# Kernel optimization log

Hardware: AMD Instinct MI355X
Metric: run time of the kernel (lower is better)

Reference implementation:

```python
import jax, jax.numpy as jnp
import numpy as np

H = 16  # num_heads
D = 64  # head_dim


def setup_inputs() -> dict:
    key = jax.random.key(0)
    ks = jax.random.split(key, 9)
    B, S, E = 2, 2048, 1024
    scale = 1.0 / np.sqrt(E)
    return {
        "hidden_states": jax.random.normal(ks[0], (B, S, E), jnp.float32),
        "bias": jax.random.normal(ks[1], (1, H, S, S), jnp.float32) * 0.02,
        "Wq": jax.random.normal(ks[2], (E, E), jnp.float32) * scale,
        "bq": jax.random.normal(ks[3], (E,), jnp.float32) * 0.02,
        "Wk": jax.random.normal(ks[4], (E, E), jnp.float32) * scale,
        "bk": jax.random.normal(ks[5], (E,), jnp.float32) * 0.02,
        "Wv": jax.random.normal(ks[6], (E, E), jnp.float32) * scale,
        "bv": jax.random.normal(ks[7], (E,), jnp.float32) * 0.02,
        "Wo": jax.random.normal(ks[8], (E, E), jnp.float32) * scale,
    }


def _split_heads(x, B, S):
    # (B, S, E) -> (B, H, S, D)
    return x.reshape(B, S, H, D).transpose(0, 2, 1, 3)


def reference(hidden_states, bias, Wq, bq, Wk, bk, Wv, bv, Wo):
    B, S, E = hidden_states.shape
    # nn.Linear: y = x @ W^T + b
    q = _split_heads(hidden_states @ Wq.T + bq, B, S)
    k = _split_heads(hidden_states @ Wk.T + bk, B, S)
    v = _split_heads(hidden_states @ Wv.T + bv, B, S)
    scores = jnp.einsum("bhqd,bhkd->bhqk", q, k) / jnp.sqrt(jnp.asarray(D, q.dtype))
    scores = scores + bias  # bias [1,H,S,S] broadcasts over batch (matches .repeat)
    attn = jax.nn.softmax(scores, axis=-1)
    out = jnp.einsum("bhqk,bhkd->bhqd", attn, v)
    out = out.transpose(0, 2, 1, 3).reshape(B, S, E)
    return out @ Wo.T
```

## Files before the change

kernel.cpp:

```cpp
#include <hip/hip_runtime.h>
#include <hip/hip_bf16.h>


typedef __attribute__((ext_vector_type(8))) __bf16 bf16x8;
typedef __attribute__((ext_vector_type(4))) float f32x4;

__device__ __forceinline__ void gl2lds16(const void* g, void* l) {
    __builtin_amdgcn_global_load_lds(
        (const __attribute__((address_space(1))) void*)g,
        (__attribute__((address_space(3))) void*)l, 16, 0, 0);
}

__global__ __launch_bounds__(256) void prep(
    const float* __restrict__ hs, const float* __restrict__ Wq,
    const float* __restrict__ Wk, const float* __restrict__ Wv,
    const float* __restrict__ Wo,
    __bf16* __restrict__ hsb, __bf16* __restrict__ wqb, __bf16* __restrict__ wkb,
    __bf16* __restrict__ wvb, __bf16* __restrict__ wohb, __bf16* __restrict__ wolb)
{
    size_t i = (size_t)blockIdx.x * 256 + threadIdx.x;
    const float* s; __bf16 *d1, *d2 = nullptr; size_t off;
    if (i < 1048576)      { s = hs; d1 = hsb; off = i; }
    else if (i < 1310720) { s = Wq; d1 = wqb; off = i - 1048576; }
    else if (i < 1572864) { s = Wk; d1 = wkb; off = i - 1310720; }
    else if (i < 1835008) { s = Wv; d1 = wvb; off = i - 1572864; }
    else                  { s = Wo; d1 = wohb; d2 = wolb; off = i - 1835008; }
    float4 v = *(const float4*)(s + off * 4);
    union { __bf16 b[4]; uint2 u; } ph;
    ph.b[0] = (__bf16)v.x; ph.b[1] = (__bf16)v.y;
    ph.b[2] = (__bf16)v.z; ph.b[3] = (__bf16)v.w;
    *(uint2*)(d1 + off * 4) = ph.u;
    if (d2) {
        union { __bf16 b[4]; uint2 u; } pl;
        pl.b[0] = (__bf16)(v.x - (float)ph.b[0]);
        pl.b[1] = (__bf16)(v.y - (float)ph.b[1]);
        pl.b[2] = (__bf16)(v.z - (float)ph.b[2]);
        pl.b[3] = (__bf16)(v.w - (float)ph.b[3]);
        *(uint2*)(d2 + off * 4) = pl.u;
    }
}

__global__ __launch_bounds__(256, 3) void gemm_qkv(
    const __bf16* __restrict__ hsb, const __bf16* __restrict__ wqb,
    const __bf16* __restrict__ wkb, const __bf16* __restrict__ wvb,
    const float* __restrict__ bq, const float* __restrict__ bk, const float* __restrict__ bv,
    __bf16* __restrict__ qo, __bf16* __restrict__ ko, __bf16* __restrict__ vTo)
{
    __shared__ alignas(16) __bf16 As[128][32];
    __shared__ alignas(16) __bf16 Ws[128][32];
    const int tid = threadIdx.x;
    const int w = tid >> 6, lane = tid & 63, quad = lane >> 4, l = lane & 15;
    const int blk = blockIdx.x;
    const int proj = blk >> 8;
    const int loc = blk & 255;
    int bm, bn;
    const __bf16 *Ap, *Wp; const float* bp;
    if (proj == 0)      { Ap = hsb; Wp = wqb; bp = bq; bm = (loc >> 3) << 7; bn = (loc & 7) << 7; }
    else if (proj == 1) { Ap = hsb; Wp = wkb; bp = bk; bm = (loc >> 3) << 7; bn = (loc & 7) << 7; }
    else                { Ap = wvb; Wp = hsb; bp = bv; bm = (loc & 7) << 7; bn = (loc >> 3) << 7; }
    const int wm = (w >> 1) << 6, wn = (w & 1) << 6;
    const int seg_r = lane >> 2, seg_c = (lane & 3) << 3;

    f32x4 acc[4][4];
#pragma unroll
    for (int i = 0; i < 4; ++i)
#pragma unroll
        for (int j = 0; j < 4; ++j) acc[i][j] = f32x4{0.f, 0.f, 0.f, 0.f};

    for (int k0 = 0; k0 < 1024; k0 += 32) {
        __syncthreads();
#pragma unroll
        for (int j = 0; j < 2; ++j) {
            int seg = w * 2 + j;
            int row = seg * 16 + seg_r;
            gl2lds16(Ap + (size_t)(bm + row) * 1024 + k0 + seg_c,
                     (char*)As + seg * 1024 + lane * 16);
            gl2lds16(Wp + (size_t)(bn + row) * 1024 + k0 + seg_c,
                     (char*)Ws + seg * 1024 + lane * 16);
        }
        __syncthreads();
        bf16x8 af[4], bfr[4];
#pragma unroll
        for (int t = 0; t < 4; ++t) {
            af[t]  = *(const bf16x8*)&As[wm + t * 16 + l][quad * 8];
            bfr[t] = *(const bf16x8*)&Ws[wn + t * 16 + l][quad * 8];
        }
#pragma unroll
        for (int mt = 0; mt < 4; ++mt)
#pragma unroll
            for (int nt = 0; nt < 4; ++nt)
                acc[mt][nt] = __builtin_amdgcn_mfma_f32_16x16x32_bf16(
                    af[mt], bfr[nt], acc[mt][nt], 0, 0, 0);
    }

    if (proj < 2) {
        __bf16* dst = proj ? ko : qo;
        const float scale = proj ? 1.0f : 0.125f;
        float bcol[4];
#pragma unroll
        for (int nt = 0; nt < 4; ++nt) bcol[nt] = bp[bn + wn + nt * 16 + l];
#pragma unroll
        for (int mt = 0; mt < 4; ++mt)
#pragma unroll
            for (int r = 0; r < 4; ++r) {
                int m = bm + wm + mt * 16 + quad * 4 + r;
                int b_ = m >> 11, s = m & 2047;
#pragma unroll
                for (int nt = 0; nt < 4; ++nt) {
                    int n = bn + wn + nt * 16 + l;
                    int h = n >> 6, d = n & 63;
                    dst[(((size_t)(b_ * 16 + h) * 2048 + s) << 6) + d] =
                        (__bf16)((acc[mt][nt][r] + bcol[nt]) * scale);
                }
            }
    } else {
#pragma unroll
        for (int mt = 0; mt < 4; ++mt)
#pragma unroll
            for (int r = 0; r < 4; ++r) {
                int im = bm + wm + mt * 16 + quad * 4 + r;
                int h = im >> 6, d = im & 63;
                float bm_ = bp[im];
#pragma unroll
                for (int nt = 0; nt < 4; ++nt) {
                    int in = bn + wn + nt * 16 + l;
                    int b_ = in >> 11, s = in & 2047;
                    vTo[(((size_t)(b_ * 16 + h) * 64 + d) << 11) + s] =
                        (__bf16)(acc[mt][nt][r] + bm_);
                }
            }
    }
}

__global__ __launch_bounds__(256, 2) void flash_attn_mfma(
    const __bf16* __restrict__ q, const __bf16* __restrict__ k,
    const __bf16* __restrict__ vT, const float* __restrict__ bias,
    __bf16* __restrict__ attn_hi, __bf16* __restrict__ attn_lo)
{
    constexpr int S = 2048;
    constexpr int NT = S / 64;
    __shared__ alignas(16) unsigned char smem[50176];
    __bf16 (*Ps)[68] = (__bf16(*)[68])(smem + 32768);

    const int tid = threadIdx.x;
    const int b = blockIdx.x, h = blockIdx.y, qt = blockIdx.z;
    const int bh = b * 16 + h;
    const int q0 = qt * 128;
    const int w = tid >> 6, lane = tid & 63, quad = lane >> 4, l = lane & 15;

    const __bf16* Kp0 = k + (size_t)bh * S * 64;
    const __bf16* Vp0 = vT + (size_t)bh * 64 * S;
    const float*  Bp0 = bias + (size_t)h * S * S + (size_t)q0 * S;

    {
        const __bf16* Qp = q + ((size_t)bh * S + q0) * 64;
#pragma unroll
        for (int j = 0; j < 4; ++j) {
            int P = (w * 4 + j) * 64 + lane;
            int row = P >> 3, pblk = P & 7;
            int lblk = pblk ^ (row & 7);
            gl2lds16(Qp + row * 64 + lblk * 8, (char*)smem + 32768 + (size_t)P * 16);
        }
#pragma unroll
        for (int j = 0; j < 2; ++j) {
            int P = (w * 2 + j) * 64 + lane;
            int row = P >> 3, pblk = P & 7;
            int lblk = pblk ^ (row & 7);
            gl2lds16(Kp0 + row * 64 + lblk * 8,        (char*)smem + (size_t)P * 16);
            gl2lds16(Vp0 + (size_t)row * S + lblk * 8, (char*)smem + 16384 + (size_t)P * 16);
        }
    }

    f32x4 pf[2][4];
#pragma unroll
    for (int rt = 0; rt < 2; ++rt)
#pragma unroll
        for (int r = 0; r < 4; ++r) {
            const float* bp = Bp0 + (size_t)(w * 32 + rt * 16 + quad * 4 + r) * S + l;
#pragma unroll
            for (int ct = 0; ct < 4; ++ct) pf[rt][ct][r] = bp[ct * 16];
        }

    __syncthreads();

    bf16x8 qf[2][2];
    {
        const __bf16 (*Qs)[64] = (const __bf16(*)[64])(smem + 32768);
#pragma unroll
        for (int rt = 0; rt < 2; ++rt)
#pragma unroll
            for (int ks = 0; ks < 2; ++ks) {
                int row = w * 32 + rt * 16 + l;
                qf[rt][ks] = *(const bf16x8*)&Qs[row][((ks * 4 + quad) ^ (row & 7)) * 8];
            }
    }
    __syncthreads();

    float l_[2][4];
    f32x4 o_[2][4];
#pragma unroll
    for (int rt = 0; rt < 2; ++rt)
#pragma unroll
        for (int r = 0; r < 4; ++r) {
            l_[rt][r] = 0.0f;
            o_[rt][r] = f32x4{0.f, 0.f, 0.f, 0.f};
        }

    for (int kt = 0; kt < NT; ++kt) {
        const int cur = kt & 1;
        const __bf16 (*Ks)[64]  = (const __bf16(*)[64])(smem + cur * 8192);
        const __bf16 (*VTs)[64] = (const __bf16(*)[64])(smem + 16384 + cur * 8192);

        f32x4 sc[2][4];
#pragma unroll
        for (int rt = 0; rt < 2; ++rt)
#pragma unroll
            for (int ct = 0; ct < 4; ++ct) sc[rt][ct] = pf[rt][ct];

        if (kt + 1 < NT) {
            const __bf16* Kt = Kp0 + (kt + 1) * 64 * 64;
            const __bf16* Vt = Vp0 + (kt + 1) * 64;
            char* Kd = (char*)smem + (cur ^ 1) * 8192;
            char* Vd = (char*)smem + 16384 + (cur ^ 1) * 8192;
#pragma unroll
            for (int j = 0; j < 2; ++j) {
                int P = (w * 2 + j) * 64 + lane;
                int row = P >> 3, pblk = P & 7;
                int lblk = pblk ^ (row & 7);
                gl2lds16(Kt + row * 64 + lblk * 8,        Kd + (size_t)P * 16);
                gl2lds16(Vt + (size_t)row * S + lblk * 8, Vd + (size_t)P * 16);
            }
            const float* Bn = Bp0 + (kt + 1) * 64;
#pragma unroll
            for (int rt = 0; rt < 2; ++rt)
#pragma unroll
                for (int r = 0; r < 4; ++r) {
                    const float* bp = Bn + (size_t)(w * 32 + rt * 16 + quad * 4 + r) * S + l;
#pragma unroll
                    for (int ct = 0; ct < 4; ++ct) pf[rt][ct][r] = bp[ct * 16];
                }
        }

        __builtin_amdgcn_s_setprio(1);
#pragma unroll
        for (int ct = 0; ct < 4; ++ct) {
            int krow = ct * 16 + l;
            bf16x8 b0 = *(const bf16x8*)&Ks[krow][((0 + quad) ^ (l & 7)) * 8];
            bf16x8 b1 = *(const bf16x8*)&Ks[krow][((4 + quad) ^ (l & 7)) * 8];
            sc[0][ct] = __builtin_amdgcn_mfma_f32_16x16x32_bf16(qf[0][0], b0, sc[0][ct], 0, 0, 0);
            sc[0][ct] = __builtin_amdgcn_mfma_f32_16x16x32_bf16(qf[0][1], b1, sc[0][ct], 0, 0, 0);
            sc[1][ct] = __builtin_amdgcn_mfma_f32_16x16x32_bf16(qf[1][0], b0, sc[1][ct], 0, 0, 0);
            sc[1][ct] = __builtin_amdgcn_mfma_f32_16x16x32_bf16(qf[1][1], b1, sc[1][ct], 0, 0, 0);
        }
        __builtin_amdgcn_s_setprio(0);

#pragma unroll
        for (int rt = 0; rt < 2; ++rt)
#pragma unroll
            for (int r = 0; r < 4; ++r) {
                int row = w * 32 + rt * 16 + quad * 4 + r;
                float ps = 0.f;
#pragma unroll
                for (int ct = 0; ct < 4; ++ct) {
                    float p = __expf(sc[rt][ct][r] - 8.0f);
                    Ps[row][ct * 16 + l] = (__bf16)p;
                    ps += p;
                }
                l_[rt][r] += ps;
            }

        __builtin_amdgcn_s_setprio(1);
#pragma unroll
        for (int ks = 0; ks < 2; ++ks) {
            bf16x8 pa0 = *(const bf16x8*)&Ps[w * 32 + l][ks * 32 + quad * 8];
            bf16x8 pa1 = *(const bf16x8*)&Ps[w * 32 + 16 + l][ks * 32 + quad * 8];
#pragma unroll
            for (int dt = 0; dt < 4; ++dt) {
                bf16x8 vb = *(const bf16x8*)&VTs[dt * 16 + l][((ks * 4 + quad) ^ (l & 7)) * 8];
                o_[0][dt] = __builtin_amdgcn_mfma_f32_16x16x32_bf16(pa0, vb, o_[0][dt], 0, 0, 0);
                o_[1][dt] = __builtin_amdgcn_mfma_f32_16x16x32_bf16(pa1, vb, o_[1][dt], 0, 0, 0);
            }
        }
        __builtin_amdgcn_s_setprio(0);

        __syncthreads();
    }

#pragma unroll
    for (int rt = 0; rt < 2; ++rt)
#pragma unroll
        for (int r = 0; r < 4; ++r) {
            float ps = l_[rt][r];
            ps += __shfl_xor(ps, 1);
            ps += __shfl_xor(ps, 2);
            ps += __shfl_xor(ps, 4);
            ps += __shfl_xor(ps, 8);
            float linv = 1.0f / ps;
            int row = q0 + w * 32 + rt * 16 + quad * 4 + r;
            size_t base = (size_t)(b * S + row) * 1024 + h * 64;
#pragma unroll
            for (int dt = 0; dt < 4; ++dt) {
                float x = o_[rt][dt][r] * linv;
                __bf16 hi = (__bf16)x;
                attn_hi[base + dt * 16 + l] = hi;
                attn_lo[base + dt * 16 + l] = (__bf16)(x - (float)hi);
            }
        }
}

__global__ __launch_bounds__(256, 3) void gemm_out(
    const __bf16* __restrict__ ah, const __bf16* __restrict__ al,
    const __bf16* __restrict__ wh, const __bf16* __restrict__ wl,
    float* __restrict__ C)
{
    __shared__ alignas(16) __bf16 Ah[64][32], Al[64][32];
    __shared__ alignas(16) __bf16 Wh[128][32], Wl[128][32];
    const int tid = threadIdx.x;
    const int w = tid >> 6, lane = tid & 63, quad = lane >> 4, l = lane & 15;
    const int bm = (int)(blockIdx.x >> 3) << 6;
    const int bn = (int)(blockIdx.x & 7) << 7;
    const int wm = (w >> 1) << 5, wn = (w & 1) << 6;
    const int seg_r = lane >> 2, seg_c = (lane & 3) << 3;

    f32x4 acc[2][4];
#pragma unroll
    for (int i = 0; i < 2; ++i)
#pragma unroll
        for (int j = 0; j < 4; ++j) acc[i][j] = f32x4{0.f, 0.f, 0.f, 0.f};

    for (int k0 = 0; k0 < 1024; k0 += 32) {
        __syncthreads();
        {
            int row = w * 16 + seg_r;
            gl2lds16(ah + (size_t)(bm + row) * 1024 + k0 + seg_c,
                     (char*)Ah + w * 1024 + lane * 16);
            gl2lds16(al + (size_t)(bm + row) * 1024 + k0 + seg_c,
                     (char*)Al + w * 1024 + lane * 16);
#pragma unroll
            for (int j = 0; j < 2; ++j) {
                int seg = w * 2 + j;
                int wrow = seg * 16 + seg_r;
                gl2lds16(wh + (size_t)(bn + wrow) * 1024 + k0 + seg_c,
                         (char*)Wh + seg * 1024 + lane * 16);
                gl2lds16(wl + (size_t)(bn + wrow) * 1024 + k0 + seg_c,
                         (char*)Wl + seg * 1024 + lane * 16);
            }
        }
        __syncthreads();
        bf16x8 ahf[2], alf[2], whf[4], wlf[4];
#pragma unroll
        for (int t = 0; t < 2; ++t) {
            ahf[t] = *(const bf16x8*)&Ah[wm + t * 16 + l][quad * 8];
            alf[t] = *(const bf16x8*)&Al[wm + t * 16 + l][quad * 8];
        }
#pragma unroll
        for (int t = 0; t < 4; ++t) {
            whf[t] = *(const bf16x8*)&Wh[wn + t * 16 + l][quad * 8];
            wlf[t] = *(const bf16x8*)&Wl[wn + t * 16 + l][quad * 8];
        }
#pragma unroll
        for (int mt = 0; mt < 2; ++mt)
#pragma unroll
            for (int nt = 0; nt < 4; ++nt) {
                acc[mt][nt] = __builtin_amdgcn_mfma_f32_16x16x32_bf16(ahf[mt], whf[nt], acc[mt][nt], 0, 0, 0);
                acc[mt][nt] = __builtin_amdgcn_mfma_f32_16x16x32_bf16(ahf[mt], wlf[nt], acc[mt][nt], 0, 0, 0);
                acc[mt][nt] = __builtin_amdgcn_mfma_f32_16x16x32_bf16(alf[mt], whf[nt], acc[mt][nt], 0, 0, 0);
            }
    }

#pragma unroll
    for (int mt = 0; mt < 2; ++mt)
#pragma unroll
        for (int r = 0; r < 4; ++r) {
            int m = bm + wm + mt * 16 + quad * 4 + r;
#pragma unroll
            for (int nt = 0; nt < 4; ++nt)
                C[(size_t)m * 1024 + bn + wn + nt * 16 + l] = acc[mt][nt][r];
        }
}

extern "C" void kernel_launch(void* const* d_in, const int* in_sizes, int n_in,
                              void* d_out, int out_size, void* d_ws, size_t ws_size,
                              hipStream_t stream) {
    const float* hs   = (const float*)d_in[0];
    const float* bias = (const float*)d_in[1];
    const float* Wq   = (const float*)d_in[2];
    const float* bq   = (const float*)d_in[3];
    const float* Wk   = (const float*)d_in[4];
    const float* bk   = (const float*)d_in[5];
    const float* Wv   = (const float*)d_in[6];
    const float* bv   = (const float*)d_in[7];
    const float* Wo   = (const float*)d_in[8];
    float* out = (float*)d_out;
    char* ws = (char*)d_ws;

    __bf16* attn_hi = (__bf16*)(ws);
    __bf16* attn_lo = (__bf16*)(ws + ((size_t) 8 << 20));
    __bf16* qb      = (__bf16*)(ws + ((size_t)16 << 20));
    __bf16* kb      = (__bf16*)(ws + ((size_t)24 << 20));
    __bf16* vTb     = (__bf16*)(ws + ((size_t)32 << 20));
    __bf16* hsb     = (__bf16*)(ws + ((size_t)40 << 20));
    __bf16* wqb     = (__bf16*)(ws + ((size_t)48 << 20));
    __bf16* wkb     = (__bf16*)(ws + ((size_t)50 << 20));
    __bf16* wvb     = (__bf16*)(ws + ((size_t)52 << 20));
    __bf16* wohb    = (__bf16*)(ws + ((size_t)54 << 20));
    __bf16* wolb    = (__bf16*)(ws + ((size_t)56 << 20));

    prep<<<8192, 256, 0, stream>>>(hs, Wq, Wk, Wv, Wo, hsb, wqb, wkb, wvb, wohb, wolb);

    gemm_qkv<<<768, 256, 0, stream>>>(hsb, wqb, wkb, wvb, bq, bk, bv, qb, kb, vTb);

    dim3 fg(2, 16, 16);
    flash_attn_mfma<<<fg, 256, 0, stream>>>(qb, kb, vTb, bias, attn_hi, attn_lo);

    gemm_out<<<512, 256, 0, stream>>>(attn_hi, attn_lo, wohb, wolb, out);
}
```

Baseline: 508.8 us.

## Process both batches per block to share bias tile loads in flash attention

```diff
diff --git a/kernel.cpp b/kernel.cpp
--- a/kernel.cpp
+++ b/kernel.cpp
@@ -140,167 +140,166 @@
     constexpr int S = 2048;
     constexpr int NT = S / 64;
     __shared__ alignas(16) unsigned char smem[50176];
-    __bf16 (*Ps)[68] = (__bf16(*)[68])(smem + 32768);
 
     const int tid = threadIdx.x;
-    const int b = blockIdx.x, h = blockIdx.y, qt = blockIdx.z;
-    const int bh = b * 16 + h;
-    const int q0 = qt * 128;
+    const int h = blockIdx.x, qt = blockIdx.y;
+    const int q0 = qt * 64;
     const int w = tid >> 6, lane = tid & 63, quad = lane >> 4, l = lane & 15;
 
-    const __bf16* Kp0 = k + (size_t)bh * S * 64;
-    const __bf16* Vp0 = vT + (size_t)bh * 64 * S;
-    const float*  Bp0 = bias + (size_t)h * S * S + (size_t)q0 * S;
-
-    {
-        const __bf16* Qp = q + ((size_t)bh * S + q0) * 64;
-#pragma unroll
-        for (int j = 0; j < 4; ++j) {
-            int P = (w * 4 + j) * 64 + lane;
-            int row = P >> 3, pblk = P & 7;
-            int lblk = pblk ^ (row & 7);
-            gl2lds16(Qp + row * 64 + lblk * 8, (char*)smem + 32768 + (size_t)P * 16);
-        }
+    const float* Bp0 = bias + (size_t)h * S * S + (size_t)q0 * S;
+
+#pragma unroll
+    for (int b = 0; b < 2; ++b) {
+        const __bf16* Qp = q + ((size_t)(b * 16 + h) * S + q0) * 64;
+        const __bf16* Kp = k + (size_t)(b * 16 + h) * S * 64;
+        const __bf16* Vp = vT + (size_t)(b * 16 + h) * 64 * S;
 #pragma unroll
         for (int j = 0; j < 2; ++j) {
             int P = (w * 2 + j) * 64 + lane;
             int row = P >> 3, pblk = P & 7;
             int lblk = pblk ^ (row & 7);
-            gl2lds16(Kp0 + row * 64 + lblk * 8,        (char*)smem + (size_t)P * 16);
-            gl2lds16(Vp0 + (size_t)row * S + lblk * 8, (char*)smem + 16384 + (size_t)P * 16);
-        }
-    }
-
-    f32x4 pf[2][4];
-#pragma unroll
-    for (int rt = 0; rt < 2; ++rt)
-#pragma unroll
-        for (int r = 0; r < 4; ++r) {
-            const float* bp = Bp0 + (size_t)(w * 32 + rt * 16 + quad * 4 + r) * S + l;
-#pragma unroll
-            for (int ct = 0; ct < 4; ++ct) pf[rt][ct][r] = bp[ct * 16];
-        }
+            gl2lds16(Qp + row * 64 + lblk * 8,
+                     (char*)smem + 32768 + b * 8192 + (size_t)P * 16);
+            gl2lds16(Kp + row * 64 + lblk * 8,
+                     (char*)smem + b * 8192 + (size_t)P * 16);
+            gl2lds16(Vp + (size_t)row * S + lblk * 8,
+                     (char*)smem + 16384 + b * 8192 + (size_t)P * 16);
+        }
+    }
+
+    f32x4 pf[4];
+#pragma unroll
+    for (int r = 0; r < 4; ++r) {
+        const float* bp = Bp0 + (size_t)(w * 16 + quad * 4 + r) * S + l;
+#pragma unroll
+        for (int ct = 0; ct < 4; ++ct) pf[ct][r] = bp[ct * 16];
+    }
 
     __syncthreads();
 
     bf16x8 qf[2][2];
-    {
-        const __bf16 (*Qs)[64] = (const __bf16(*)[64])(smem + 32768);
-#pragma unroll
-        for (int rt = 0; rt < 2; ++rt)
-#pragma unroll
-            for (int ks = 0; ks < 2; ++ks) {
-                int row = w * 32 + rt * 16 + l;
-                qf[rt][ks] = *(const bf16x8*)&Qs[row][((ks * 4 + quad) ^ (row & 7)) * 8];
-            }
+#pragma unroll
+    for (int b = 0; b < 2; ++b) {
+        const __bf16 (*Qs)[64] = (const __bf16(*)[64])(smem + 32768 + b * 8192);
+        int row = w * 16 + l;
+#pragma unroll
+        for (int ks = 0; ks < 2; ++ks)
+            qf[b][ks] = *(const bf16x8*)&Qs[row][((ks * 4 + quad) ^ (l & 7)) * 8];
     }
     __syncthreads();
 
     float l_[2][4];
     f32x4 o_[2][4];
 #pragma unroll
-    for (int rt = 0; rt < 2; ++rt)
+    for (int b = 0; b < 2; ++b)
 #pragma unroll
         for (int r = 0; r < 4; ++r) {
-            l_[rt][r] = 0.0f;
-            o_[rt][r] = f32x4{0.f, 0.f, 0.f, 0.f};
+            l_[b][r] = 0.0f;
+            o_[b][r] = f32x4{0.f, 0.f, 0.f, 0.f};
         }
 
     for (int kt = 0; kt < NT; ++kt) {
-        const int cur = kt & 1;
-        const __bf16 (*Ks)[64]  = (const __bf16(*)[64])(smem + cur * 8192);
-        const __bf16 (*VTs)[64] = (const __bf16(*)[64])(smem + 16384 + cur * 8192);
-
         f32x4 sc[2][4];
 #pragma unroll
-        for (int rt = 0; rt < 2; ++rt)
-#pragma unroll
-            for (int ct = 0; ct < 4; ++ct) sc[rt][ct] = pf[rt][ct];
+        for (int b = 0; b < 2; ++b)
+#pragma unroll
+            for (int ct = 0; ct < 4; ++ct) sc[b][ct] = pf[ct];
 
         if (kt + 1 < NT) {
-            const __bf16* Kt = Kp0 + (kt + 1) * 64 * 64;
-            const __bf16* Vt = Vp0 + (kt + 1) * 64;
-            char* Kd = (char*)smem + (cur ^ 1) * 8192;
-            char* Vd = (char*)smem + 16384 + (cur ^ 1) * 8192;
-#pragma unroll
-            for (int j = 0; j < 2; ++j) {
-                int P = (w * 2 + j) * 64 + lane;
-                int row = P >> 3, pblk = P & 7;
-                int lblk = pblk ^ (row & 7);
-                gl2lds16(Kt + row * 64 + lblk * 8,        Kd + (size_t)P * 16);
-                gl2lds16(Vt + (size_t)row * S + lblk * 8, Vd + (size_t)P * 16);
-            }
             const float* Bn = Bp0 + (kt + 1) * 64;
 #pragma unroll
-            for (int rt = 0; rt < 2; ++rt)
-#pragma unroll
-                for (int r = 0; r < 4; ++r) {
-                    const float* bp = Bn + (size_t)(w * 32 + rt * 16 + quad * 4 + r) * S + l;
-#pragma unroll
-                    for (int ct = 0; ct < 4; ++ct) pf[rt][ct][r] = bp[ct * 16];
-                }
+            for (int r = 0; r < 4; ++r) {
+                const float* bp = Bn + (size_t)(w * 16 + quad * 4 + r) * S + l;
+#pragma unroll
+                for (int ct = 0; ct < 4; ++ct) pf[ct][r] = bp[ct * 16];
+            }
         }
 
         __builtin_amdgcn_s_setprio(1);
 #pragma unroll
-        for (int ct = 0; ct < 4; ++ct) {
-            int krow = ct * 16 + l;
-            bf16x8 b0 = *(const bf16x8*)&Ks[krow][((0 + quad) ^ (l & 7)) * 8];
-            bf16x8 b1 = *(const bf16x8*)&Ks[krow][((4 + quad) ^ (l & 7)) * 8];
-            sc[0][ct] = __builtin_amdgcn_mfma_f32_16x16x32_bf16(qf[0][0], b0, sc[0][ct], 0, 0, 0);
-            sc[0][ct] = __builtin_amdgcn_mfma_f32_16x16x32_bf16(qf[0][1], b1, sc[0][ct], 0, 0, 0);
-            sc[1][ct] = __builtin_amdgcn_mfma_f32_16x16x32_bf16(qf[1][0], b0, sc[1][ct], 0, 0, 0);
-            sc[1][ct] = __builtin_amdgcn_mfma_f32_16x16x32_bf16(qf[1][1], b1, sc[1][ct], 0, 0, 0);
+        for (int b = 0; b < 2; ++b) {
+            const __bf16 (*Ks)[64] = (const __bf16(*)[64])(smem + b * 8192);
+#pragma unroll
+            for (int ct = 0; ct < 4; ++ct) {
+                int krow = ct * 16 + l;
+                bf16x8 k0 = *(const bf16x8*)&Ks[krow][((0 + quad) ^ (l & 7)) * 8];
+                bf16x8 k1 = *(const bf16x8*)&Ks[krow][((4 + quad) ^ (l & 7)) * 8];
+                sc[b][ct] = __builtin_amdgcn_mfma_f32_16x16x32_bf16(qf[b][0], k0, sc[b][ct], 0, 0, 0);
+                sc[b][ct] = __builtin_amdgcn_mfma_f32_16x16x32_bf16(qf[b][1], k1, sc[b][ct], 0, 0, 0);
+            }
         }
         __builtin_amdgcn_s_setprio(0);
 
 #pragma unroll
-        for (int rt = 0; rt < 2; ++rt)
+        for (int b = 0; b < 2; ++b) {
+            __bf16 (*Ps)[68] = (__bf16(*)[68])(smem + 32768 + b * 8704);
 #pragma unroll
             for (int r = 0; r < 4; ++r) {
-                int row = w * 32 + rt * 16 + quad * 4 + r;
+                int row = w * 16 + quad * 4 + r;
                 float ps = 0.f;
 #pragma unroll
                 for (int ct = 0; ct < 4; ++ct) {
-                    float p = __expf(sc[rt][ct][r] - 8.0f);
+                    float p = __expf(sc[b][ct][r] - 8.0f);
                     Ps[row][ct * 16 + l] = (__bf16)p;
                     ps += p;
                 }
-                l_[rt][r] += ps;
-            }
+                l_[b][r] += ps;
+            }
+        }
 
         __builtin_amdgcn_s_setprio(1);
 #pragma unroll
-        for (int ks = 0; ks < 2; ++ks) {
-            bf16x8 pa0 = *(const bf16x8*)&Ps[w * 32 + l][ks * 32 + quad * 8];
-            bf16x8 pa1 = *(const bf16x8*)&Ps[w * 32 + 16 + l][ks * 32 + quad * 8];
-#pragma unroll
-            for (int dt = 0; dt < 4; ++dt) {
-                bf16x8 vb = *(const bf16x8*)&VTs[dt * 16 + l][((ks * 4 + quad) ^ (l & 7)) * 8];
-                o_[0][dt] = __builtin_amdgcn_mfma_f32_16x16x32_bf16(pa0, vb, o_[0][dt], 0, 0, 0);
-                o_[1][dt] = __builtin_amdgcn_mfma_f32_16x16x32_bf16(pa1, vb, o_[1][dt], 0, 0, 0);
+        for (int b = 0; b < 2; ++b) {
+            const __bf16 (*Ps)[68] = (const __bf16(*)[68])(smem + 32768 + b * 8704);
+            const __bf16 (*VTs)[64] = (const __bf16(*)[64])(smem + 16384 + b * 8192);
+#pragma unroll
+            for (int ks = 0; ks < 2; ++ks) {
+                bf16x8 pa = *(const bf16x8*)&Ps[w * 16 + l][ks * 32 + quad * 8];
+#pragma unroll
+                for (int dt = 0; dt < 4; ++dt) {
+                    bf16x8 vb = *(const bf16x8*)&VTs[dt * 16 + l][((ks * 4 + quad) ^ (l & 7)) * 8];
+                    o_[b][dt] = __builtin_amdgcn_mfma_f32_16x16x32_bf16(pa, vb, o_[b][dt], 0, 0, 0);
+                }
             }
         }
         __builtin_amdgcn_s_setprio(0);
 
-        __syncthreads();
-    }
-
-#pragma unroll
-    for (int rt = 0; rt < 2; ++rt)
+        if (kt + 1 < NT) {
+            __syncthreads();
+#pragma unroll
+            for (int b = 0; b < 2; ++b) {
+                const __bf16* Kp = k + (size_t)(b * 16 + h) * S * 64 + (size_t)(kt + 1) * 64 * 64;
+                const __bf16* Vp = vT + (size_t)(b * 16 + h) * 64 * S + (size_t)(kt + 1) * 64;
+#pragma unroll
+                for (int j = 0; j < 2; ++j) {
+                    int P = (w * 2 + j) * 64 + lane;
+                    int row = P >> 3, pblk = P & 7;
+                    int lblk = pblk ^ (row & 7);
+                    gl2lds16(Kp + row * 64 + lblk * 8,
+                             (char*)smem + b * 8192 + (size_t)P * 16);
+                    gl2lds16(Vp + (size_t)row * S + lblk * 8,
+                             (char*)smem + 16384 + b * 8192 + (size_t)P * 16);
+                }
+            }
+            __syncthreads();
+        }
+    }
+
+#pragma unroll
+    for (int b = 0; b < 2; ++b)
 #pragma unroll
         for (int r = 0; r < 4; ++r) {
-            float ps = l_[rt][r];
+            float ps = l_[b][r];
             ps += __shfl_xor(ps, 1);
             ps += __shfl_xor(ps, 2);
             ps += __shfl_xor(ps, 4);
             ps += __shfl_xor(ps, 8);
             float linv = 1.0f / ps;
-            int row = q0 + w * 32 + rt * 16 + quad * 4 + r;
+            int row = q0 + w * 16 + quad * 4 + r;
             size_t base = (size_t)(b * S + row) * 1024 + h * 64;
 #pragma unroll
             for (int dt = 0; dt < 4; ++dt) {
-                float x = o_[rt][dt][r] * linv;
+                float x = o_[b][dt][r] * linv;
                 __bf16 hi = (__bf16)x;
                 attn_hi[base + dt * 16 + l] = hi;
                 attn_lo[base + dt * 16 + l] = (__bf16)(x - (float)hi);
@@ -410,7 +409,7 @@
 
     gemm_qkv<<<768, 256, 0, stream>>>(hsb, wqb, wkb, wvb, bq, bk, bv, qb, kb, vTb);
 
-    dim3 fg(2, 16, 16);
+    dim3 fg(16, 32);
     flash_attn_mfma<<<fg, 256, 0, stream>>>(qb, kb, vTb, bias, attn_hi, attn_lo);
 
     gemm_out<<<512, 256, 0, stream>>>(attn_hi, attn_lo, wohb, wolb, out);
```

New measurement: 502.8 us. Within noise of the previous version (-1.2%).
